# Performance work log

Measured on AMD Instinct MI355X. Metric: run time of the kernel, lower is better.

## Reference

```python
import jax, jax.numpy as jnp
import numpy as np

HEADS = 8
DIM_HEAD = 64
SCALE = DIM_HEAD ** -0.5


def setup_inputs() -> dict:
    key = jax.random.key(0)
    k1, k2, k3, k4 = jax.random.split(key, 4)
    b, dim, l = 4, 256, 2048
    hidden = HEADS * DIM_HEAD  # 512
    x = jax.random.normal(k1, (b, dim, l), dtype=jnp.float32)
    w_qkv = jax.random.normal(k2, (3 * hidden, dim), dtype=jnp.float32) * (dim ** -0.5)
    w_out = jax.random.normal(k3, (dim, hidden), dtype=jnp.float32) * (hidden ** -0.5)
    b_out = jax.random.normal(k4, (dim,), dtype=jnp.float32) * 0.01
    return {"x": x, "w_qkv": w_qkv, "w_out": w_out, "b_out": b_out}


def reference(x, w_qkv, w_out, b_out):
    b, c, l = x.shape
    hidden = HEADS * DIM_HEAD
    # 1x1 conv == pointwise linear over channels
    qkv = jnp.einsum('oc,bcl->bol', w_qkv, x)  # [b, 3*hidden, l]
    q, k, v = jnp.split(qkv, 3, axis=1)
    def to_heads(t):
        return t.reshape(b, HEADS, DIM_HEAD, l)  # b h d l
    q, k, v = to_heads(q), to_heads(k), to_heads(v)
    q = q * SCALE
    sim = jnp.einsum('bhdi,bhdj->bhij', q, k)      # [b, h, l, l]
    attn = jax.nn.softmax(sim, axis=-1)
    out = jnp.einsum('bhij,bhdj->bhid', attn, v)   # [b, h, l, d]
    out = out.transpose(0, 1, 3, 2).reshape(b, hidden, l)  # b (h d) l
    return jnp.einsum('oc,bcl->bol', w_out, out) + b_out[None, :, None]
```

## Files before the change

### kernel.cpp

```cpp
#include <hip/hip_runtime.h>
#include <math.h>

#define Bn   4
#define Cc   256
#define Ll   2048
#define Hh   8
#define Dd   64
#define HID  512
#define OQKV 1536

#define QSCALE 0.18033688011112042f
#define ESHIFT 4.328085122666891f

typedef _Float16 half4v __attribute__((ext_vector_type(4)));
typedef _Float16 half8v __attribute__((ext_vector_type(8)));
typedef __fp16   fp16x2 __attribute__((ext_vector_type(2)));
typedef float    f32x16 __attribute__((ext_vector_type(16)));
typedef unsigned uint2v __attribute__((ext_vector_type(2)));

__device__ __forceinline__ void gload_lds16(const _Float16* g, _Float16* l) {
  __builtin_amdgcn_global_load_lds(
      (const __attribute__((address_space(1))) void*)g,
      (__attribute__((address_space(3))) void*)l, 16, 0, 0);
}

__global__ __launch_bounds__(256) void conv_xTw(const float* __restrict__ x,
                                                const float* __restrict__ wqkv,
                                                const float* __restrict__ wout,
                                                _Float16* __restrict__ xT,
                                                _Float16* __restrict__ wqkvh,
                                                _Float16* __restrict__ wouth) {
  __shared__ _Float16 T[64][72];
  const int l0 = blockIdx.x * 64, c0 = blockIdx.y * 64, bz = blockIdx.z;
  const int t = threadIdx.x;
  {
    int gid = (((blockIdx.z * gridDim.y + blockIdx.y) * gridDim.x + blockIdx.x) << 8) + t;
    int nthr = (gridDim.x * gridDim.y * gridDim.z) << 8;
    for (int i = gid; i < OQKV * Cc; i += nthr) {
      float v = wqkv[i];
      if (i < HID * Cc) v *= QSCALE;
      wqkvh[i] = (_Float16)v;
    }
    for (int i = gid; i < Cc * HID; i += nthr) wouth[i] = (_Float16)wout[i];
  }
  const float* xb = x + ((size_t)bz * Cc + c0) * Ll + l0;
  {
    int cl = t >> 2;
    int lq = (t & 3) * 16;
#pragma unroll
    for (int i = 0; i < 16; i += 4) {
      float4 v = *(const float4*)&xb[(size_t)cl * Ll + lq + i];
      T[lq + i + 0][cl] = (_Float16)v.x;
      T[lq + i + 1][cl] = (_Float16)v.y;
      T[lq + i + 2][cl] = (_Float16)v.z;
      T[lq + i + 3][cl] = (_Float16)v.w;
    }
  }
  __syncthreads();
  {
    int ll = t >> 2;
    int cq = (t & 3) * 16;
    _Float16* dst = xT + ((size_t)bz * Ll + l0 + ll) * Cc + c0 + cq;
    *(half8v*)&dst[0] = *(const half8v*)&T[ll][cq];
    *(half8v*)&dst[8] = *(const half8v*)&T[ll][cq + 8];
  }
}

template <int MODE>
__global__ __launch_bounds__(256) void gemm_f16(
    const _Float16* __restrict__ A, const _Float16* __restrict__ B,
    const float* __restrict__ bias, void* __restrict__ C, int M, int K) {
  __shared__ _Float16 As[128][64];
  __shared__ _Float16 Bs[128][64];
  const int bz = blockIdx.z;
  const int m0 = blockIdx.y * 128, n0 = blockIdx.x * 128;
  const int t = threadIdx.x;
  const int w = t >> 6, lane = t & 63, lid = lane & 31, lh = lane >> 5;
  const int mw = (w >> 1) * 64, nw = (w & 1) * 64;
  const _Float16* Bb = B + (size_t)bz * (size_t)Ll * K;

  const int srow = lane >> 3;
  const int sgr  = ((lane & 7) ^ srow) << 3;

  f32x16 acc[2][2];
#pragma unroll
  for (int a = 0; a < 2; ++a)
#pragma unroll
    for (int b2 = 0; b2 < 2; ++b2)
#pragma unroll
      for (int r = 0; r < 16; ++r) acc[a][b2][r] = 0.0f;

  for (int k0 = 0; k0 < K; k0 += 64) {
#pragma unroll
    for (int q = 0; q < 4; ++q) {
      const int r0 = (q * 4 + w) * 8;
      const int row = r0 + srow;
      gload_lds16(&A[(size_t)(m0 + row) * K + k0 + sgr], &As[r0][0]);
      gload_lds16(&Bb[(size_t)(n0 + row) * K + k0 + sgr], &Bs[r0][0]);
    }
    __syncthreads();
    const int rk = lid & 7;
#pragma unroll
    for (int kq = 0; kq < 4; ++kq) {
      half8v af[2], bf[2];
#pragma unroll
      for (int ms = 0; ms < 2; ++ms)
        af[ms] = *(const half8v*)&As[mw + ms * 32 + lid][((2 * kq + lh) ^ rk) << 3];
#pragma unroll
      for (int ns = 0; ns < 2; ++ns)
        bf[ns] = *(const half8v*)&Bs[nw + ns * 32 + lid][((2 * kq + lh) ^ rk) << 3];
#pragma unroll
      for (int ms = 0; ms < 2; ++ms)
#pragma unroll
        for (int ns = 0; ns < 2; ++ns)
          acc[ms][ns] = __builtin_amdgcn_mfma_f32_32x32x16_f16(af[ms], bf[ns], acc[ms][ns], 0, 0, 0);
    }
    __syncthreads();
  }
#pragma unroll
  for (int ms = 0; ms < 2; ++ms)
#pragma unroll
    for (int ns = 0; ns < 2; ++ns)
#pragma unroll
      for (int r = 0; r < 16; ++r) {
        int row = m0 + mw + ms * 32 + (r & 3) + 8 * (r >> 2) + 4 * lh;
        int col = n0 + nw + ns * 32 + lid;
        float v = acc[ms][ns][r];
        if (MODE == 1) {
          ((float*)C)[((size_t)bz * M + row) * Ll + col] = v + bias[row];
        } else {
          ((_Float16*)C)[((size_t)bz * M + row) * Ll + col] = (_Float16)v;
        }
      }
}

__device__ inline unsigned pkrtz(float a, float b) {
  union { fp16x2 h; unsigned u; } x;
  x.h = __builtin_amdgcn_cvt_pkrtz(a, b);
  return x.u;
}

__global__ __launch_bounds__(512, 4) void attn_f16(const _Float16* __restrict__ qkv,
                                                   _Float16* __restrict__ aoutT) {
  const int n = blockIdx.x;
  const int xcd = n & 7;
  const int x = (n >> 3) & 15;
  const int gs = n >> 7;
  const int g = gs * 8 + xcd;
  const int h = g & 7, b = g >> 3;
  const int i0 = x * 128;

  const int t = threadIdx.x;
  const int w = t >> 6, lane = t & 63, lid = lane & 31, lh = lane >> 5;
  const int wg = w & 3;
  const int wj = w >> 2;
  const _Float16* qb = qkv + ((size_t)b * OQKV + h * Dd) * Ll;
  const _Float16* kb = qb + (size_t)HID * Ll;
  const _Float16* vb = qb + (size_t)(2 * HID) * Ll;

  __shared__ __align__(16) char lds_raw[55296];
  _Float16 (*Qs)[72]     = (_Float16 (*)[72])(lds_raw);
  _Float16 (*Ks)[64][72] = (_Float16 (*)[64][72])(lds_raw + 18432);
  _Float16 (*Vs)[64][72] = (_Float16 (*)[64][72])(lds_raw + 36864);

  {
    int il = ((t >> 8) << 6) + (t & 15) * 4;
    int dl = ((t >> 4) & 15) * 4;
    int cc = dl >> 3, cs = dl & 7;
    half4v rows[4];
#pragma unroll
    for (int r = 0; r < 4; ++r)
      rows[r] = *(const half4v*)&qb[(size_t)(dl + r) * Ll + i0 + il];
#pragma unroll
    for (int c = 0; c < 4; ++c) {
      half4v o;
      o[0] = rows[0][c]; o[1] = rows[1][c]; o[2] = rows[2][c]; o[3] = rows[3][c];
      int row = il + c;
      *(half4v*)&Qs[row][((cc ^ ((row >> 2) & 7)) << 3) | cs] = o;
    }
  }

  const bool isK = t < 256;
  const int ts = isK ? t : t - 256;
  const int kjl = (ts & 15) * 4, kdl = (ts >> 4) * 4;
  const int kcc = kdl >> 3, kcs = kdl & 7;
  const int vdl = ts >> 2, vjl = (ts & 3) * 16;

  if (isK) {
    half4v rows[4];
#pragma unroll
    for (int r = 0; r < 4; ++r)
      rows[r] = *(const half4v*)&kb[(size_t)(kdl + r) * Ll + kjl];
#pragma unroll
    for (int c = 0; c < 4; ++c) {
      half4v o;
      o[0] = rows[0][c]; o[1] = rows[1][c]; o[2] = rows[2][c]; o[3] = rows[3][c];
      int row = kjl + c;
      *(half4v*)&Ks[0][row][((kcc ^ ((row >> 2) & 7)) << 3) | kcs] = o;
    }
  } else {
    *(half8v*)&Vs[0][vdl][vjl]     = *(const half8v*)&vb[(size_t)vdl * Ll + vjl];
    *(half8v*)&Vs[0][vdl][vjl + 8] = *(const half8v*)&vb[(size_t)vdl * Ll + vjl + 8];
  }
  __syncthreads();

  const int key = (lid >> 2) & 7;
  half8v qf[4];
#pragma unroll
  for (int kq = 0; kq < 4; ++kq)
    qf[kq] = *(const half8v*)&Qs[32 * wg + lid][((2 * kq + lh) ^ key) << 3];

  float lsum = 0.0f;
  f32x16 oacc[2];
#pragma unroll
  for (int ds = 0; ds < 2; ++ds)
#pragma unroll
    for (int r = 0; r < 16; ++r) oacc[ds][r] = 0.0f;

  const int krow = wj * 32 + lid;

  for (int j0 = 0; j0 < Ll; j0 += 64) {
    const int cur = (j0 >> 6) & 1;
    const int nj = j0 + 64;
    const bool more = nj < Ll;

    half4v krows[4];
    half8v vr0, vr1;
    if (more) {
      if (isK) {
#pragma unroll
        for (int r = 0; r < 4; ++r)
          krows[r] = *(const half4v*)&kb[(size_t)(kdl + r) * Ll + nj + kjl];
      } else {
        vr0 = *(const half8v*)&vb[(size_t)vdl * Ll + nj + vjl];
        vr1 = *(const half8v*)&vb[(size_t)vdl * Ll + nj + vjl + 8];
      }
    }

    f32x16 s;
#pragma unroll
    for (int r = 0; r < 16; ++r) s[r] = -ESHIFT;
    __builtin_amdgcn_s_setprio(1);
#pragma unroll
    for (int kq = 0; kq < 4; ++kq) {
      half8v kf = *(const half8v*)&Ks[cur][krow][((2 * kq + lh) ^ key) << 3];
      s = __builtin_amdgcn_mfma_f32_32x32x16_f16(kf, qf[kq], s, 0, 0, 0);
    }
    __builtin_amdgcn_s_setprio(0);
    unsigned W[8];
#pragma unroll
    for (int q = 0; q < 4; ++q) {
      float p0 = __builtin_amdgcn_exp2f(s[4 * q + 0]);
      float p1 = __builtin_amdgcn_exp2f(s[4 * q + 1]);
      float p2 = __builtin_amdgcn_exp2f(s[4 * q + 2]);
      float p3 = __builtin_amdgcn_exp2f(s[4 * q + 3]);
      lsum += (p0 + p1) + (p2 + p3);
      W[2 * q]     = pkrtz(p0, p1);
      W[2 * q + 1] = pkrtz(p2, p3);
    }
#pragma unroll
    for (int f = 0; f < 2; ++f) {
      uint2v r02 = __builtin_amdgcn_permlane32_swap(W[4 * f + 0], W[4 * f + 2], false, false);
      uint2v r13 = __builtin_amdgcn_permlane32_swap(W[4 * f + 1], W[4 * f + 3], false, false);
      union { unsigned u[4]; half8v hv; } pu;
      pu.u[0] = r02[0];
      pu.u[1] = r13[0];
      pu.u[2] = r02[1];
      pu.u[3] = r13[1];
      const int jq = 2 * wj + f;
      __builtin_amdgcn_s_setprio(1);
#pragma unroll
      for (int ds = 0; ds < 2; ++ds) {
        half8v vf = *(const half8v*)&Vs[cur][ds * 32 + lid][jq * 16 + 8 * lh];
        oacc[ds] = __builtin_amdgcn_mfma_f32_32x32x16_f16(vf, pu.hv, oacc[ds], 0, 0, 0);
      }
      __builtin_amdgcn_s_setprio(0);
    }

    if (more) {
      const int nb = cur ^ 1;
      if (isK) {
#pragma unroll
        for (int c = 0; c < 4; ++c) {
          half4v o;
          o[0] = krows[0][c]; o[1] = krows[1][c]; o[2] = krows[2][c]; o[3] = krows[3][c];
          int row = kjl + c;
          *(half4v*)&Ks[nb][row][((kcc ^ ((row >> 2) & 7)) << 3) | kcs] = o;
        }
      } else {
        *(half8v*)&Vs[nb][vdl][vjl]     = vr0;
        *(half8v*)&Vs[nb][vdl][vjl + 8] = vr1;
      }
      __syncthreads();
    }
  }

  lsum += __shfl_xor(lsum, 32);
  __syncthreads();
  float* red = (float*)lds_raw;
  const int rbase = ((wg << 6) + lane) * 33;
  if (wj == 1) {
#pragma unroll
    for (int ds = 0; ds < 2; ++ds)
#pragma unroll
      for (int r = 0; r < 16; ++r) red[rbase + ds * 16 + r] = oacc[ds][r];
    red[rbase + 32] = lsum;
  }
  __syncthreads();
  if (wj == 0) {
#pragma unroll
    for (int ds = 0; ds < 2; ++ds)
#pragma unroll
      for (int r = 0; r < 16; ++r) oacc[ds][r] += red[rbase + ds * 16 + r];
    lsum += red[rbase + 32];
    float inv = 1.0f / lsum;
    _Float16* dst = aoutT + ((size_t)b * Ll + i0 + 32 * wg + lid) * HID + h * Dd;
#pragma unroll
    for (int ds = 0; ds < 2; ++ds)
#pragma unroll
      for (int g2 = 0; g2 < 4; ++g2) {
        int d = ds * 32 + 8 * g2 + 4 * lh;
        half4v o;
#pragma unroll
        for (int c = 0; c < 4; ++c) o[c] = (_Float16)(oacc[ds][4 * g2 + c] * inv);
        *(half4v*)&dst[d] = o;
      }
  }
}

extern "C" void kernel_launch(void* const* d_in, const int* in_sizes, int n_in,
                              void* d_out, int out_size, void* d_ws, size_t ws_size,
                              hipStream_t stream) {
  const float* x     = (const float*)d_in[0];
  const float* w_qkv = (const float*)d_in[1];
  const float* w_out = (const float*)d_in[2];
  const float* b_out = (const float*)d_in[3];
  float* out = (float*)d_out;

  char* ws = (char*)d_ws;
  _Float16* xT     = (_Float16*)(ws);
  _Float16* wqkvh  = (_Float16*)(ws + 4194304);
  _Float16* wouth  = (_Float16*)(ws + 4980736);
  _Float16* qkvh   = (_Float16*)(ws + 5242880);
  _Float16* aoutT  = (_Float16*)(ws + 30408704);

  dim3 blk(256);
  conv_xTw<<<dim3(Ll / 64, Cc / 64, Bn), blk, 0, stream>>>(x, w_qkv, w_out, xT, wqkvh, wouth);
  gemm_f16<0><<<dim3(Ll / 128, OQKV / 128, Bn), blk, 0, stream>>>(
      wqkvh, xT, nullptr, qkvh, OQKV, Cc);
  attn_f16<<<dim3(512, 1, 1), dim3(512), 0, stream>>>(qkvh, aoutT);
  gemm_f16<1><<<dim3(Ll / 128, Cc / 128, Bn), blk, 0, stream>>>(
      wouth, aoutT, b_out, out, Cc, HID);
}
```

Measured before the change: 143.1 us.

## Fuse fp32-to-fp16 conversion and transpose into GEMM tile loads, drop prep kernel

New measurement: 155.6 us. 8.7% more time.

```diff
diff --git a/kernel.cpp b/kernel.cpp
--- a/kernel.cpp
+++ b/kernel.cpp
@@ -24,61 +24,108 @@
       (__attribute__((address_space(3))) void*)l, 16, 0, 0);
 }
 
-__global__ __launch_bounds__(256) void conv_xTw(const float* __restrict__ x,
-                                                const float* __restrict__ wqkv,
-                                                const float* __restrict__ wout,
-                                                _Float16* __restrict__ xT,
-                                                _Float16* __restrict__ wqkvh,
-                                                _Float16* __restrict__ wouth) {
-  __shared__ _Float16 T[64][72];
-  const int l0 = blockIdx.x * 64, c0 = blockIdx.y * 64, bz = blockIdx.z;
+__global__ __launch_bounds__(256) void gemm_qkv(const float* __restrict__ wqkv,
+                                                const float* __restrict__ x,
+                                                _Float16* __restrict__ qkvh) {
+  __shared__ _Float16 As[128][72];
+  __shared__ _Float16 Bs[128][72];
+  const int bz = blockIdx.z;
+  const int m0 = blockIdx.y * 128, n0 = blockIdx.x * 128;
   const int t = threadIdx.x;
-  {
-    int gid = (((blockIdx.z * gridDim.y + blockIdx.y) * gridDim.x + blockIdx.x) << 8) + t;
-    int nthr = (gridDim.x * gridDim.y * gridDim.z) << 8;
-    for (int i = gid; i < OQKV * Cc; i += nthr) {
-      float v = wqkv[i];
-      if (i < HID * Cc) v *= QSCALE;
-      wqkvh[i] = (_Float16)v;
-    }
-    for (int i = gid; i < Cc * HID; i += nthr) wouth[i] = (_Float16)wout[i];
-  }
-  const float* xb = x + ((size_t)bz * Cc + c0) * Ll + l0;
-  {
-    int cl = t >> 2;
-    int lq = (t & 3) * 16;
-#pragma unroll
-    for (int i = 0; i < 16; i += 4) {
-      float4 v = *(const float4*)&xb[(size_t)cl * Ll + lq + i];
-      T[lq + i + 0][cl] = (_Float16)v.x;
-      T[lq + i + 1][cl] = (_Float16)v.y;
-      T[lq + i + 2][cl] = (_Float16)v.z;
-      T[lq + i + 3][cl] = (_Float16)v.w;
-    }
-  }
-  __syncthreads();
-  {
-    int ll = t >> 2;
-    int cq = (t & 3) * 16;
-    _Float16* dst = xT + ((size_t)bz * Ll + l0 + ll) * Cc + c0 + cq;
-    *(half8v*)&dst[0] = *(const half8v*)&T[ll][cq];
-    *(half8v*)&dst[8] = *(const half8v*)&T[ll][cq + 8];
-  }
-}
-
-template <int MODE>
-__global__ __launch_bounds__(256) void gemm_f16(
-    const _Float16* __restrict__ A, const _Float16* __restrict__ B,
-    const float* __restrict__ bias, void* __restrict__ C, int M, int K) {
-  __shared__ _Float16 As[128][64];
+  const int w = t >> 6, lane = t & 63, lid = lane & 31, lh = lane >> 5;
+  const int mw = (w >> 1) * 64, nw = (w & 1) * 64;
+  const float* xb = x + (size_t)bz * Cc * Ll;
+
+  const int arow = t >> 1, acb = (t & 1) * 4;
+  const float ascale = (m0 + arow) < HID ? QSCALE : 1.0f;
+  const int akey = (arow >> 2) & 7;
+  const int bcg = t & 15, blg = t >> 4;
+
+  f32x16 acc[2][2];
+#pragma unroll
+  for (int a = 0; a < 2; ++a)
+#pragma unroll
+    for (int b2 = 0; b2 < 2; ++b2)
+#pragma unroll
+      for (int r = 0; r < 16; ++r) acc[a][b2][r] = 0.0f;
+
+  for (int k0 = 0; k0 < Cc; k0 += 64) {
+#pragma unroll
+    for (int i = 0; i < 4; ++i) {
+      const int cc = acb + i;
+      const float* src = &wqkv[(size_t)(m0 + arow) * Cc + k0 + cc * 8];
+      float4 f0 = *(const float4*)&src[0];
+      float4 f1 = *(const float4*)&src[4];
+      half8v hv;
+      hv[0] = (_Float16)(f0.x * ascale); hv[1] = (_Float16)(f0.y * ascale);
+      hv[2] = (_Float16)(f0.z * ascale); hv[3] = (_Float16)(f0.w * ascale);
+      hv[4] = (_Float16)(f1.x * ascale); hv[5] = (_Float16)(f1.y * ascale);
+      hv[6] = (_Float16)(f1.z * ascale); hv[7] = (_Float16)(f1.w * ascale);
+      *(half8v*)&As[arow][(cc ^ akey) << 3] = hv;
+    }
+#pragma unroll
+    for (int p = 0; p < 2; ++p) {
+      const int lbase = blg * 4 + p * 64;
+      float4 rows[4];
+#pragma unroll
+      for (int r = 0; r < 4; ++r)
+        rows[r] = *(const float4*)&xb[(size_t)(k0 + bcg * 4 + r) * Ll + n0 + lbase];
+#pragma unroll
+      for (int j = 0; j < 4; ++j) {
+        half4v o;
+        o[0] = (_Float16)rows[0][j]; o[1] = (_Float16)rows[1][j];
+        o[2] = (_Float16)rows[2][j]; o[3] = (_Float16)rows[3][j];
+        const int row = lbase + j;
+        const int cc = bcg >> 1, cs = (bcg & 1) * 4;
+        *(half4v*)&Bs[row][(((cc ^ ((row >> 2) & 7)) << 3) | cs)] = o;
+      }
+    }
+    __syncthreads();
+    const int key = (lid >> 2) & 7;
+#pragma unroll
+    for (int kq = 0; kq < 4; ++kq) {
+      half8v af[2], bf[2];
+#pragma unroll
+      for (int ms = 0; ms < 2; ++ms)
+        af[ms] = *(const half8v*)&As[mw + ms * 32 + lid][((2 * kq + lh) ^ key) << 3];
+#pragma unroll
+      for (int ns = 0; ns < 2; ++ns)
+        bf[ns] = *(const half8v*)&Bs[nw + ns * 32 + lid][((2 * kq + lh) ^ key) << 3];
+#pragma unroll
+      for (int ms = 0; ms < 2; ++ms)
+#pragma unroll
+        for (int ns = 0; ns < 2; ++ns)
+          acc[ms][ns] = __builtin_amdgcn_mfma_f32_32x32x16_f16(af[ms], bf[ns], acc[ms][ns], 0, 0, 0);
+    }
+    __syncthreads();
+  }
+#pragma unroll
+  for (int ms = 0; ms < 2; ++ms)
+#pragma unroll
+    for (int ns = 0; ns < 2; ++ns)
+#pragma unroll
+      for (int r = 0; r < 16; ++r) {
+        int row = m0 + mw + ms * 32 + (r & 3) + 8 * (r >> 2) + 4 * lh;
+        int col = n0 + nw + ns * 32 + lid;
+        qkvh[((size_t)bz * OQKV + row) * Ll + col] = (_Float16)acc[ms][ns][r];
+      }
+}
+
+__global__ __launch_bounds__(256) void gemm_out(const float* __restrict__ wout,
+                                                const _Float16* __restrict__ aoutT,
+                                                const float* __restrict__ bias,
+                                                float* __restrict__ out) {
+  __shared__ _Float16 As[128][72];
   __shared__ _Float16 Bs[128][64];
   const int bz = blockIdx.z;
   const int m0 = blockIdx.y * 128, n0 = blockIdx.x * 128;
   const int t = threadIdx.x;
   const int w = t >> 6, lane = t & 63, lid = lane & 31, lh = lane >> 5;
   const int mw = (w >> 1) * 64, nw = (w & 1) * 64;
-  const _Float16* Bb = B + (size_t)bz * (size_t)Ll * K;
-
+  const _Float16* Bb = aoutT + (size_t)bz * Ll * HID;
+
+  const int arow = t >> 1, acb = (t & 1) * 4;
+  const int akey = (arow >> 2) & 7;
   const int srow = lane >> 3;
   const int sgr  = ((lane & 7) ^ srow) << 3;
 
@@ -90,22 +137,34 @@
 #pragma unroll
       for (int r = 0; r < 16; ++r) acc[a][b2][r] = 0.0f;
 
-  for (int k0 = 0; k0 < K; k0 += 64) {
+  for (int k0 = 0; k0 < HID; k0 += 64) {
+#pragma unroll
+    for (int i = 0; i < 4; ++i) {
+      const int cc = acb + i;
+      const float* src = &wout[(size_t)(m0 + arow) * HID + k0 + cc * 8];
+      float4 f0 = *(const float4*)&src[0];
+      float4 f1 = *(const float4*)&src[4];
+      half8v hv;
+      hv[0] = (_Float16)f0.x; hv[1] = (_Float16)f0.y;
+      hv[2] = (_Float16)f0.z; hv[3] = (_Float16)f0.w;
+      hv[4] = (_Float16)f1.x; hv[5] = (_Float16)f1.y;
+      hv[6] = (_Float16)f1.z; hv[7] = (_Float16)f1.w;
+      *(half8v*)&As[arow][(cc ^ akey) << 3] = hv;
+    }
 #pragma unroll
     for (int q = 0; q < 4; ++q) {
       const int r0 = (q * 4 + w) * 8;
-      const int row = r0 + srow;
-      gload_lds16(&A[(size_t)(m0 + row) * K + k0 + sgr], &As[r0][0]);
-      gload_lds16(&Bb[(size_t)(n0 + row) * K + k0 + sgr], &Bs[r0][0]);
+      gload_lds16(&Bb[(size_t)(n0 + r0 + srow) * HID + k0 + sgr], &Bs[r0][0]);
     }
     __syncthreads();
+    const int key = (lid >> 2) & 7;
     const int rk = lid & 7;
 #pragma unroll
     for (int kq = 0; kq < 4; ++kq) {
       half8v af[2], bf[2];
 #pragma unroll
       for (int ms = 0; ms < 2; ++ms)
-        af[ms] = *(const half8v*)&As[mw + ms * 32 + lid][((2 * kq + lh) ^ rk) << 3];
+        af[ms] = *(const half8v*)&As[mw + ms * 32 + lid][((2 * kq + lh) ^ key) << 3];
 #pragma unroll
       for (int ns = 0; ns < 2; ++ns)
         bf[ns] = *(const half8v*)&Bs[nw + ns * 32 + lid][((2 * kq + lh) ^ rk) << 3];
@@ -125,12 +184,7 @@
       for (int r = 0; r < 16; ++r) {
         int row = m0 + mw + ms * 32 + (r & 3) + 8 * (r >> 2) + 4 * lh;
         int col = n0 + nw + ns * 32 + lid;
-        float v = acc[ms][ns][r];
-        if (MODE == 1) {
-          ((float*)C)[((size_t)bz * M + row) * Ll + col] = v + bias[row];
-        } else {
-          ((_Float16*)C)[((size_t)bz * M + row) * Ll + col] = (_Float16)v;
-        }
+        out[((size_t)bz * Cc + row) * Ll + col] = acc[ms][ns][r] + bias[row];
       }
 }
 
@@ -338,17 +392,10 @@
   float* out = (float*)d_out;
 
   char* ws = (char*)d_ws;
-  _Float16* xT     = (_Float16*)(ws);
-  _Float16* wqkvh  = (_Float16*)(ws + 4194304);
-  _Float16* wouth  = (_Float16*)(ws + 4980736);
-  _Float16* qkvh   = (_Float16*)(ws + 5242880);
-  _Float16* aoutT  = (_Float16*)(ws + 30408704);
-
-  dim3 blk(256);
-  conv_xTw<<<dim3(Ll / 64, Cc / 64, Bn), blk, 0, stream>>>(x, w_qkv, w_out, xT, wqkvh, wouth);
-  gemm_f16<0><<<dim3(Ll / 128, OQKV / 128, Bn), blk, 0, stream>>>(
-      wqkvh, xT, nullptr, qkvh, OQKV, Cc);
+  _Float16* qkvh  = (_Float16*)(ws);
+  _Float16* aoutT = (_Float16*)(ws + 25165824);
+
+  gemm_qkv<<<dim3(Ll / 128, OQKV / 128, Bn), dim3(256), 0, stream>>>(w_qkv, x, qkvh);
   attn_f16<<<dim3(512, 1, 1), dim3(512), 0, stream>>>(qkvh, aoutT);
-  gemm_f16<1><<<dim3(Ll / 128, Cc / 128, Bn), blk, 0, stream>>>(
-      wouth, aoutT, b_out, out, Cc, HID);
-}
+  gemm_out<<<dim3(Ll / 128, Cc / 128, Bn), dim3(256), 0, stream>>>(w_out, aoutT, b_out, out);
+}
```

## Fuse all four stages into one cooperative persistent kernel with grid syncs

Applied to the files above, without the earlier changes.

Result: slower. 318.4 us (+122.4%).

```diff
diff --git a/kernel.cpp b/kernel.cpp
--- a/kernel.cpp
+++ b/kernel.cpp
@@ -1,5 +1,8 @@
 #include <hip/hip_runtime.h>
+#include <hip/hip_cooperative_groups.h>
 #include <math.h>
+
+namespace cg = cooperative_groups;
 
 #define Bn   4
 #define Cc   256
@@ -22,6 +25,328 @@
   __builtin_amdgcn_global_load_lds(
       (const __attribute__((address_space(1))) void*)g,
       (__attribute__((address_space(3))) void*)l, 16, 0, 0);
+}
+
+__device__ inline unsigned pkrtz(float a, float b) {
+  union { fp16x2 h; unsigned u; } v;
+  v.h = __builtin_amdgcn_cvt_pkrtz(a, b);
+  return v.u;
+}
+
+__global__ __launch_bounds__(512, 4) void mega(
+    const float* __restrict__ x, const float* __restrict__ wqkv,
+    const float* __restrict__ wout, const float* __restrict__ bias,
+    float* __restrict__ out, _Float16* __restrict__ xT,
+    _Float16* __restrict__ wqkvh, _Float16* __restrict__ wouth,
+    _Float16* __restrict__ qkvh, _Float16* __restrict__ aoutT) {
+  cg::grid_group gg = cg::this_grid();
+  const int bid = blockIdx.x;
+  const int t = threadIdx.x;
+  __shared__ __align__(16) char lds[55296];
+
+  {
+    _Float16 (*T)[72] = (_Float16 (*)[72])lds;
+    const int l0 = (bid & 31) * 64, c0 = ((bid >> 5) & 3) * 64, bz = bid >> 7;
+    {
+      int gid = (bid << 9) + t;
+      for (int i = gid; i < OQKV * Cc; i += 262144) {
+        float v = wqkv[i];
+        if (i < HID * Cc) v *= QSCALE;
+        wqkvh[i] = (_Float16)v;
+      }
+      for (int i = gid; i < Cc * HID; i += 262144) wouth[i] = (_Float16)wout[i];
+    }
+    const float* xb = x + ((size_t)bz * Cc + c0) * Ll + l0;
+    const int cl = t >> 3, lq = (t & 7) * 8;
+#pragma unroll
+    for (int i = 0; i < 8; i += 4) {
+      float4 v = *(const float4*)&xb[(size_t)cl * Ll + lq + i];
+      T[lq + i + 0][cl] = (_Float16)v.x;
+      T[lq + i + 1][cl] = (_Float16)v.y;
+      T[lq + i + 2][cl] = (_Float16)v.z;
+      T[lq + i + 3][cl] = (_Float16)v.w;
+    }
+    __syncthreads();
+    _Float16* dst = xT + ((size_t)bz * Ll + l0 + (t >> 3)) * Cc + c0 + (t & 7) * 8;
+    *(half8v*)dst = *(const half8v*)&T[t >> 3][(t & 7) * 8];
+  }
+  gg.sync();
+
+  {
+    _Float16 (*As)[64] = (_Float16 (*)[64])lds;
+    _Float16 (*Bs)[64] = (_Float16 (*)[64])(lds + 16384);
+    const int w = t >> 6, lane = t & 63, lid = lane & 31, lh = lane >> 5;
+    const int mw = (w & 1) * 64, nw = (w >> 1) * 32;
+    const int srow = lane >> 3, sgr = ((lane & 7) ^ srow) << 3;
+    const int rk = lid & 7;
+    for (int job = bid; job < 768; job += 512) {
+      const int bx = job & 15, rem = job >> 4;
+      const int m0 = (rem % 12) * 128, n0 = bx * 128;
+      const size_t bz = rem / 12;
+      const _Float16* Bb = xT + bz * Ll * Cc;
+      f32x16 acc[2];
+#pragma unroll
+      for (int a = 0; a < 2; ++a)
+#pragma unroll
+        for (int r = 0; r < 16; ++r) acc[a][r] = 0.0f;
+      for (int k0 = 0; k0 < Cc; k0 += 64) {
+#pragma unroll
+        for (int q = 0; q < 2; ++q) {
+          const int r0 = (q * 8 + w) * 8;
+          gload_lds16(&wqkvh[(size_t)(m0 + r0 + srow) * Cc + k0 + sgr], &As[r0][0]);
+          gload_lds16(&Bb[(size_t)(n0 + r0 + srow) * Cc + k0 + sgr], &Bs[r0][0]);
+        }
+        __syncthreads();
+#pragma unroll
+        for (int kq = 0; kq < 4; ++kq) {
+          const int co = ((2 * kq + lh) ^ rk) << 3;
+          half8v af0 = *(const half8v*)&As[mw + lid][co];
+          half8v af1 = *(const half8v*)&As[mw + 32 + lid][co];
+          half8v bf  = *(const half8v*)&Bs[nw + lid][co];
+          acc[0] = __builtin_amdgcn_mfma_f32_32x32x16_f16(af0, bf, acc[0], 0, 0, 0);
+          acc[1] = __builtin_amdgcn_mfma_f32_32x32x16_f16(af1, bf, acc[1], 0, 0, 0);
+        }
+        __syncthreads();
+      }
+#pragma unroll
+      for (int ms = 0; ms < 2; ++ms)
+#pragma unroll
+        for (int r = 0; r < 16; ++r) {
+          const int row = m0 + mw + ms * 32 + (r & 3) + 8 * (r >> 2) + 4 * lh;
+          const int col = n0 + nw + lid;
+          qkvh[(bz * OQKV + row) * Ll + col] = (_Float16)acc[ms][r];
+        }
+    }
+  }
+  gg.sync();
+
+  {
+    const int n = bid;
+    const int xcd = n & 7;
+    const int xt = (n >> 3) & 15;
+    const int gs = n >> 7;
+    const int g = gs * 8 + xcd;
+    const int h = g & 7, b = g >> 3;
+    const int i0 = xt * 128;
+
+    const int w = t >> 6, lane = t & 63, lid = lane & 31, lh = lane >> 5;
+    const int wg = w & 3;
+    const int wj = w >> 2;
+    const _Float16* qb = qkvh + ((size_t)b * OQKV + h * Dd) * Ll;
+    const _Float16* kb = qb + (size_t)HID * Ll;
+    const _Float16* vb = qb + (size_t)(2 * HID) * Ll;
+
+    _Float16 (*Qs)[72]     = (_Float16 (*)[72])lds;
+    _Float16 (*Ks)[64][72] = (_Float16 (*)[64][72])(lds + 18432);
+    _Float16 (*Vs)[64][72] = (_Float16 (*)[64][72])(lds + 36864);
+
+    {
+      int il = ((t >> 8) << 6) + (t & 15) * 4;
+      int dl = ((t >> 4) & 15) * 4;
+      int cc = dl >> 3, cs = dl & 7;
+      half4v rows[4];
+#pragma unroll
+      for (int r = 0; r < 4; ++r)
+        rows[r] = *(const half4v*)&qb[(size_t)(dl + r) * Ll + i0 + il];
+#pragma unroll
+      for (int c = 0; c < 4; ++c) {
+        half4v o;
+        o[0] = rows[0][c]; o[1] = rows[1][c]; o[2] = rows[2][c]; o[3] = rows[3][c];
+        int row = il + c;
+        *(half4v*)&Qs[row][((cc ^ ((row >> 2) & 7)) << 3) | cs] = o;
+      }
+    }
+
+    const bool isK = t < 256;
+    const int ts = isK ? t : t - 256;
+    const int kjl = (ts & 15) * 4, kdl = (ts >> 4) * 4;
+    const int kcc = kdl >> 3, kcs = kdl & 7;
+    const int vdl = ts >> 2, vjl = (ts & 3) * 16;
+
+    if (isK) {
+      half4v rows[4];
+#pragma unroll
+      for (int r = 0; r < 4; ++r)
+        rows[r] = *(const half4v*)&kb[(size_t)(kdl + r) * Ll + kjl];
+#pragma unroll
+      for (int c = 0; c < 4; ++c) {
+        half4v o;
+        o[0] = rows[0][c]; o[1] = rows[1][c]; o[2] = rows[2][c]; o[3] = rows[3][c];
+        int row = kjl + c;
+        *(half4v*)&Ks[0][row][((kcc ^ ((row >> 2) & 7)) << 3) | kcs] = o;
+      }
+    } else {
+      *(half8v*)&Vs[0][vdl][vjl]     = *(const half8v*)&vb[(size_t)vdl * Ll + vjl];
+      *(half8v*)&Vs[0][vdl][vjl + 8] = *(const half8v*)&vb[(size_t)vdl * Ll + vjl + 8];
+    }
+    __syncthreads();
+
+    const int key = (lid >> 2) & 7;
+    half8v qf[4];
+#pragma unroll
+    for (int kq = 0; kq < 4; ++kq)
+      qf[kq] = *(const half8v*)&Qs[32 * wg + lid][((2 * kq + lh) ^ key) << 3];
+
+    float lsum = 0.0f;
+    f32x16 oacc[2];
+#pragma unroll
+    for (int ds = 0; ds < 2; ++ds)
+#pragma unroll
+      for (int r = 0; r < 16; ++r) oacc[ds][r] = 0.0f;
+
+    const int krow = wj * 32 + lid;
+
+    for (int j0 = 0; j0 < Ll; j0 += 64) {
+      const int cur = (j0 >> 6) & 1;
+      const int nj = j0 + 64;
+      const bool more = nj < Ll;
+
+      half4v krows[4];
+      half8v vr0, vr1;
+      if (more) {
+        if (isK) {
+#pragma unroll
+          for (int r = 0; r < 4; ++r)
+            krows[r] = *(const half4v*)&kb[(size_t)(kdl + r) * Ll + nj + kjl];
+        } else {
+          vr0 = *(const half8v*)&vb[(size_t)vdl * Ll + nj + vjl];
+          vr1 = *(const half8v*)&vb[(size_t)vdl * Ll + nj + vjl + 8];
+        }
+      }
+
+      f32x16 s;
+#pragma unroll
+      for (int r = 0; r < 16; ++r) s[r] = -ESHIFT;
+      __builtin_amdgcn_s_setprio(1);
+#pragma unroll
+      for (int kq = 0; kq < 4; ++kq) {
+        half8v kf = *(const half8v*)&Ks[cur][krow][((2 * kq + lh) ^ key) << 3];
+        s = __builtin_amdgcn_mfma_f32_32x32x16_f16(kf, qf[kq], s, 0, 0, 0);
+      }
+      __builtin_amdgcn_s_setprio(0);
+      unsigned W[8];
+#pragma unroll
+      for (int q = 0; q < 4; ++q) {
+        float p0 = __builtin_amdgcn_exp2f(s[4 * q + 0]);
+        float p1 = __builtin_amdgcn_exp2f(s[4 * q + 1]);
+        float p2 = __builtin_amdgcn_exp2f(s[4 * q + 2]);
+        float p3 = __builtin_amdgcn_exp2f(s[4 * q + 3]);
+        lsum += (p0 + p1) + (p2 + p3);
+        W[2 * q]     = pkrtz(p0, p1);
+        W[2 * q + 1] = pkrtz(p2, p3);
+      }
+#pragma unroll
+      for (int f = 0; f < 2; ++f) {
+        uint2v r02 = __builtin_amdgcn_permlane32_swap(W[4 * f + 0], W[4 * f + 2], false, false);
+        uint2v r13 = __builtin_amdgcn_permlane32_swap(W[4 * f + 1], W[4 * f + 3], false, false);
+        union { unsigned u[4]; half8v hv; } pu;
+        pu.u[0] = r02[0];
+        pu.u[1] = r13[0];
+        pu.u[2] = r02[1];
+        pu.u[3] = r13[1];
+        const int jq = 2 * wj + f;
+        __builtin_amdgcn_s_setprio(1);
+#pragma unroll
+        for (int ds = 0; ds < 2; ++ds) {
+          half8v vf = *(const half8v*)&Vs[cur][ds * 32 + lid][jq * 16 + 8 * lh];
+          oacc[ds] = __builtin_amdgcn_mfma_f32_32x32x16_f16(vf, pu.hv, oacc[ds], 0, 0, 0);
+        }
+        __builtin_amdgcn_s_setprio(0);
+      }
+
+      if (more) {
+        const int nb = cur ^ 1;
+        if (isK) {
+#pragma unroll
+          for (int c = 0; c < 4; ++c) {
+            half4v o;
+            o[0] = krows[0][c]; o[1] = krows[1][c]; o[2] = krows[2][c]; o[3] = krows[3][c];
+            int row = kjl + c;
+            *(half4v*)&Ks[nb][row][((kcc ^ ((row >> 2) & 7)) << 3) | kcs] = o;
+          }
+        } else {
+          *(half8v*)&Vs[nb][vdl][vjl]     = vr0;
+          *(half8v*)&Vs[nb][vdl][vjl + 8] = vr1;
+        }
+        __syncthreads();
+      }
+    }
+
+    lsum += __shfl_xor(lsum, 32);
+    __syncthreads();
+    float* red = (float*)lds;
+    const int rbase = ((wg << 6) + lane) * 33;
+    if (wj == 1) {
+#pragma unroll
+      for (int ds = 0; ds < 2; ++ds)
+#pragma unroll
+        for (int r = 0; r < 16; ++r) red[rbase + ds * 16 + r] = oacc[ds][r];
+      red[rbase + 32] = lsum;
+    }
+    __syncthreads();
+    if (wj == 0) {
+#pragma unroll
+      for (int ds = 0; ds < 2; ++ds)
+#pragma unroll
+        for (int r = 0; r < 16; ++r) oacc[ds][r] += red[rbase + ds * 16 + r];
+      lsum += red[rbase + 32];
+      float inv = 1.0f / lsum;
+      _Float16* dst = aoutT + ((size_t)b * Ll + i0 + 32 * wg + lid) * HID + h * Dd;
+#pragma unroll
+      for (int ds = 0; ds < 2; ++ds)
+#pragma unroll
+        for (int g2 = 0; g2 < 4; ++g2) {
+          int d = ds * 32 + 8 * g2 + 4 * lh;
+          half4v o;
+#pragma unroll
+          for (int c = 0; c < 4; ++c) o[c] = (_Float16)(oacc[ds][4 * g2 + c] * inv);
+          *(half4v*)&dst[d] = o;
+        }
+    }
+  }
+  gg.sync();
+
+  if (bid < 256) {
+    _Float16 (*As)[64] = (_Float16 (*)[64])lds;
+    _Float16 (*Bs)[64] = (_Float16 (*)[64])(lds + 8192);
+    const int w = t >> 6, lane = t & 63, lid = lane & 31, lh = lane >> 5;
+    const int mw = (w & 1) * 32, nw = (w >> 1) * 32;
+    const int srow = lane >> 3, sgr = ((lane & 7) ^ srow) << 3;
+    const int rk = lid & 7;
+    const int bx = bid & 15, by = (bid >> 4) & 3;
+    const size_t bz = bid >> 6;
+    const int m0 = by * 64, n0 = bx * 128;
+    const _Float16* Bb = aoutT + bz * Ll * HID;
+    f32x16 acc;
+#pragma unroll
+    for (int r = 0; r < 16; ++r) acc[r] = 0.0f;
+    for (int k0 = 0; k0 < HID; k0 += 64) {
+      {
+        const int r0a = w * 8;
+        gload_lds16(&wouth[(size_t)(m0 + r0a + srow) * HID + k0 + sgr], &As[r0a][0]);
+#pragma unroll
+        for (int q = 0; q < 2; ++q) {
+          const int r0 = (q * 8 + w) * 8;
+          gload_lds16(&Bb[(size_t)(n0 + r0 + srow) * HID + k0 + sgr], &Bs[r0][0]);
+        }
+      }
+      __syncthreads();
+#pragma unroll
+      for (int kq = 0; kq < 4; ++kq) {
+        const int co = ((2 * kq + lh) ^ rk) << 3;
+        half8v af = *(const half8v*)&As[mw + lid][co];
+        half8v bf = *(const half8v*)&Bs[nw + lid][co];
+        acc = __builtin_amdgcn_mfma_f32_32x32x16_f16(af, bf, acc, 0, 0, 0);
+      }
+      __syncthreads();
+    }
+#pragma unroll
+    for (int r = 0; r < 16; ++r) {
+      const int row = m0 + mw + (r & 3) + 8 * (r >> 2) + 4 * lh;
+      const int col = n0 + nw + lid;
+      out[(bz * Cc + row) * Ll + col] = acc[r] + bias[row];
+    }
+  }
 }
 
 __global__ __launch_bounds__(256) void conv_xTw(const float* __restrict__ x,
@@ -45,8 +370,7 @@
   }
   const float* xb = x + ((size_t)bz * Cc + c0) * Ll + l0;
   {
-    int cl = t >> 2;
-    int lq = (t & 3) * 16;
+    int cl = t >> 2, lq = (t & 3) * 16;
 #pragma unroll
     for (int i = 0; i < 16; i += 4) {
       float4 v = *(const float4*)&xb[(size_t)cl * Ll + lq + i];
@@ -58,8 +382,7 @@
   }
   __syncthreads();
   {
-    int ll = t >> 2;
-    int cq = (t & 3) * 16;
+    int ll = t >> 2, cq = (t & 3) * 16;
     _Float16* dst = xT + ((size_t)bz * Ll + l0 + ll) * Cc + c0 + cq;
     *(half8v*)&dst[0] = *(const half8v*)&T[ll][cq];
     *(half8v*)&dst[8] = *(const half8v*)&T[ll][cq + 8];
@@ -78,7 +401,6 @@
   const int w = t >> 6, lane = t & 63, lid = lane & 31, lh = lane >> 5;
   const int mw = (w >> 1) * 64, nw = (w & 1) * 64;
   const _Float16* Bb = B + (size_t)bz * (size_t)Ll * K;
-
   const int srow = lane >> 3;
   const int sgr  = ((lane & 7) ^ srow) << 3;
 
@@ -132,12 +454,6 @@
           ((_Float16*)C)[((size_t)bz * M + row) * Ll + col] = (_Float16)v;
         }
       }
-}
-
-__device__ inline unsigned pkrtz(float a, float b) {
-  union { fp16x2 h; unsigned u; } x;
-  x.h = __builtin_amdgcn_cvt_pkrtz(a, b);
-  return x.u;
 }
 
 __global__ __launch_bounds__(512, 4) void attn_f16(const _Float16* __restrict__ qkv,
@@ -344,11 +660,19 @@
   _Float16* qkvh   = (_Float16*)(ws + 5242880);
   _Float16* aoutT  = (_Float16*)(ws + 30408704);
 
-  dim3 blk(256);
-  conv_xTw<<<dim3(Ll / 64, Cc / 64, Bn), blk, 0, stream>>>(x, w_qkv, w_out, xT, wqkvh, wouth);
-  gemm_f16<0><<<dim3(Ll / 128, OQKV / 128, Bn), blk, 0, stream>>>(
-      wqkvh, xT, nullptr, qkvh, OQKV, Cc);
-  attn_f16<<<dim3(512, 1, 1), dim3(512), 0, stream>>>(qkvh, aoutT);
-  gemm_f16<1><<<dim3(Ll / 128, Cc / 128, Bn), blk, 0, stream>>>(
-      wouth, aoutT, b_out, out, Cc, HID);
+  void* args[] = {(void*)&x, (void*)&w_qkv, (void*)&w_out, (void*)&b_out,
+                  (void*)&out, (void*)&xT, (void*)&wqkvh, (void*)&wouth,
+                  (void*)&qkvh, (void*)&aoutT};
+  hipError_t err = hipLaunchCooperativeKernel((const void*)mega, dim3(512),
+                                              dim3(512), args, 0, stream);
+  if (err != hipSuccess) {
+    dim3 blk(256);
+    conv_xTw<<<dim3(Ll / 64, Cc / 64, Bn), blk, 0, stream>>>(x, w_qkv, w_out,
+                                                             xT, wqkvh, wouth);
+    gemm_f16<0><<<dim3(Ll / 128, OQKV / 128, Bn), blk, 0, stream>>>(
+        wqkvh, xT, nullptr, qkvh, OQKV, Cc);
+    attn_f16<<<dim3(512, 1, 1), dim3(512), 0, stream>>>(qkvh, aoutT);
+    gemm_f16<1><<<dim3(Ll / 128, Cc / 128, Bn), blk, 0, stream>>>(
+        wouth, aoutT, b_out, out, Cc, HID);
+  }
 }
```
